# Performance work log

Measured on AMD Instinct MI355X. Metric: run time of the kernel, lower is better.

Reference implementation:

```python
import jax, jax.numpy as jnp
import numpy as np


def _dnn(a, b):
    # tf.math.divide_no_nan
    safe = jnp.where(b == 0, 1.0, b)
    return jnp.where(b == 0, 0.0, a / safe)


def _safe_sqrt(x):
    # _sqrt: 0 where x == 0 (grad-safe)
    p = x > 0
    return jnp.where(p, jnp.sqrt(jnp.where(p, x, 1.0)), 0.0)


def _agg4(v):
    # mean/var/skew/kurt over last axis, using the sample skew/kurt formulas
    # from _skewness2/_kurtosis2 in the source.
    n = float(v.shape[-1])
    m = jnp.mean(v, -1)
    c = v - m[..., None]
    var = jnp.mean(c ** 2, -1)
    std = _safe_sqrt(var)
    skew = n / ((n - 1.0) * (n - 2.0)) * jnp.sum(_dnn(c, std[..., None]) ** 3, -1)
    k4 = jnp.sum(c ** 4, -1)
    k22 = jnp.sum(c ** 2, -1) ** 2
    alpha = n * (n + 1.0) * (n - 1.0) / (n - 2.0) / (n - 3.0)
    kurt = alpha * _dnn(k4, k22) - 3.0 * (n - 1.0) ** 2 / (n - 2.0) / (n - 3.0)
    return m, var, skew, kurt


def _forward(x):
    B, T, F = x.shape
    nT = float(T)

    mean = jnp.mean(x, 1)                        # [B,F]
    xc = x - mean[:, None, :]                    # x_sub_means
    var = jnp.mean(xc ** 2, 1)                   # population variance
    std = _safe_sqrt(var)
    # diff: conv kernel [0,1,-1] VALID -> d[t] = x[t+1] - x[t+2], len T-2
    xd = x[:, 1:-1, :] - x[:, 2:, :]
    xd_abs = jnp.abs(xd)

    scal = [mean,
            jnp.min(x, 1), jnp.max(x, 1),
            _safe_sqrt(jnp.mean(x ** 2, 1)),      # rms
            var, std]
    # skewness / kurtosis over time (exact formulas from source)
    skew = nT / ((nT - 1.0) * (nT - 2.0)) * jnp.sum(_dnn(xc, std[:, None, :]) ** 3, 1)
    k4 = jnp.sum(xc ** 4, 1)
    k22 = jnp.sum(xc ** 2, 1) ** 2
    alpha = nT * (nT + 1.0) * (nT - 1.0) / (nT - 2.0) / (nT - 3.0)
    kurt = alpha * _dnn(k4, k22) - 3.0 * (nT - 1.0) ** 2 / (nT - 2.0) / (nT - 3.0)
    scal += [skew, kurt,
             jnp.mean(xd, 1), jnp.sum(xd, 1), jnp.mean(xd_abs, 1),  # change stats
             jnp.sum(x ** 2, 1),                  # abs_energy
             jnp.max(jnp.abs(x), 1),              # abs_max
             jnp.sum(xd_abs, 1),                  # abs_sum_of_changes
             _safe_sqrt(jnp.sum(xd ** 2, 1))]     # cid_ce

    # quantiles (sorted) and time-based quantiles
    xs = jnp.sort(x, axis=1)
    q_idx = [round(p * T) for p in (0.25, 0.5, 0.75)]
    q = xs[:, q_idx, :]                           # [B,3,F]
    tb_idx = [min(round(p * T), T - 1) for p in (0.0, 0.25, 0.5, 0.75, 1.0)]
    tb = x[:, tb_idx, :]                          # [B,5,F]

    def count_above(sgn):
        # count_above_zero: T - count_nonzero(sign - 1) == #(sign == 1)
        return jnp.sum(sgn == 1, 1).astype(x.dtype)

    def crossings(sgn):
        return jnp.sum(sgn[:, 1:, :] != sgn[:, :-1, :], 1).astype(x.dtype)

    s_x = jnp.sign(x)
    s_c = jnp.sign(xc)
    s_tb = [jnp.sign(x - tb[:, i:i + 1, :]) for i in range(5)]
    s_q = [jnp.sign(x - q[:, i:i + 1, :]) for i in range(3)]

    scal += [count_above(s_x), count_above(s_c)] + [count_above(s) for s in s_tb]
    scal += [crossings(s_x), crossings(s_c)]
    scal += [crossings(s) for s in s_q]
    scal += [crossings(s) for s in s_tb]

    # FFT features
    fx = jnp.fft.rfft(x, axis=1)                  # [B, T//2+1, F]
    amp = jnp.transpose(jnp.abs(fx), (0, 2, 1))   # [B,F,nf]
    ang = jnp.transpose(jnp.angle(fx), (0, 2, 1))
    ratio = _dnn(amp, jnp.sum(amp, -1, keepdims=True))
    am, av, ask, aku = _agg4(amp)
    rm, rv, rsk, rku = _agg4(ratio)
    scal += [amp[:, :, 0], am, av, ask, aku, rm, rv, rsk, rku]

    # autocorrelation (lags 1..9), matching _autocorrelation:
    # ac[l] = sum_t xc[t]*xc[t+l] / (T - l) / variance
    lags = list(range(1, 10))
    ac = jnp.stack([_dnn(jnp.sum(xc[:, :T - l, :] * xc[:, l:, :], 1) / (nT - l), var)
                    for l in lags], axis=-1)      # [B,F,9]
    acm, acv, acs, ack = _agg4(ac)
    ac_rmax = _dnn(ac, jnp.max(ac, -1, keepdims=True))
    scal += [acm, acv, acs, ack]

    out = jnp.concatenate(
        [jnp.stack(scal, -1),                     # [B,F,45]
         jnp.transpose(q, (0, 2, 1)),             # [B,F,3]
         jnp.transpose(tb, (0, 2, 1)),            # [B,F,5]
         amp, ang, ratio,                         # [B,F,1025] each
         ac, ac_rmax], axis=-1)                   # [B,F,9] each
    return out                                    # [B,F,3146]


def setup_inputs() -> dict:
    key = jax.random.key(0)
    x = jax.random.normal(key, (512, 2048, 16), dtype=jnp.float32)
    return {"x": x}


def reference(x):
    return _forward(x)
```

## Files before the change

### kernel.cpp

```cpp
#include <hip/hip_runtime.h>
#include <math.h>

#define T_LEN 2048
#define NF    16
#define NTH   256
#define NOUT  3146
#define PI_F  3.14159265358979323846f

__device__ __forceinline__ float wred_sum(float v) {
  v += __shfl_down(v, 32); v += __shfl_down(v, 16); v += __shfl_down(v, 8);
  v += __shfl_down(v, 4);  v += __shfl_down(v, 2);  v += __shfl_down(v, 1);
  return v;
}
__device__ __forceinline__ float wred_min(float v) {
  v = fminf(v, __shfl_down(v, 32)); v = fminf(v, __shfl_down(v, 16)); v = fminf(v, __shfl_down(v, 8));
  v = fminf(v, __shfl_down(v, 4));  v = fminf(v, __shfl_down(v, 2));  v = fminf(v, __shfl_down(v, 1));
  return v;
}
__device__ __forceinline__ float wred_max(float v) {
  v = fmaxf(v, __shfl_down(v, 32)); v = fmaxf(v, __shfl_down(v, 16)); v = fmaxf(v, __shfl_down(v, 8));
  v = fmaxf(v, __shfl_down(v, 4));  v = fmaxf(v, __shfl_down(v, 2));  v = fmaxf(v, __shfl_down(v, 1));
  return v;
}

template<int N>
__device__ __forceinline__ void block_sum_n(float (&v)[N], float* redw, float* res, int tid) {
  const int wave = tid >> 6;
#pragma unroll
  for (int j = 0; j < N; j++) {
    float s = wred_sum(v[j]);
    if ((tid & 63) == 0) redw[j * 4 + wave] = s;
  }
  __syncthreads();
  if (tid < N) res[tid] = redw[tid * 4] + redw[tid * 4 + 1] + redw[tid * 4 + 2] + redw[tid * 4 + 3];
  __syncthreads();
}

__device__ __forceinline__ void agg4_9(const float* v, float* om, float* ov, float* os, float* ok) {
  const float fn = 9.0f;
  float s = 0.f;
#pragma unroll
  for (int i = 0; i < 9; i++) s += v[i];
  float m = s / fn;
  float c2 = 0.f, c3 = 0.f, c4 = 0.f;
#pragma unroll
  for (int i = 0; i < 9; i++) {
    float c = v[i] - m; float cc = c * c;
    c2 += cc; c3 += cc * c; c4 += cc * cc;
  }
  float var = c2 / fn;
  float sd = (var > 0.f) ? sqrtf(var) : 0.f;
  float sk = (sd > 0.f) ? fn / ((fn - 1.f) * (fn - 2.f)) * (c3 / (sd * sd * sd)) : 0.f;
  float k22 = c2 * c2;
  float al = fn * (fn + 1.f) * (fn - 1.f) / ((fn - 2.f) * (fn - 3.f));
  float ku = ((k22 > 0.f) ? al * c4 / k22 : 0.f)
             - 3.f * (fn - 1.f) * (fn - 1.f) / ((fn - 2.f) * (fn - 3.f));
  *om = m; *ov = var; *os = sk; *ok = ku;
}

__device__ __forceinline__ void hist_scan(unsigned int* U, int tid) {
  if (tid < 64) {
    const int l = tid;
    unsigned int b0 = U[4*l]   + U[256+4*l]   + U[512+4*l]   + U[768+4*l];
    unsigned int b1 = U[4*l+1] + U[256+4*l+1] + U[512+4*l+1] + U[768+4*l+1];
    unsigned int b2 = U[4*l+2] + U[256+4*l+2] + U[512+4*l+2] + U[768+4*l+2];
    unsigned int b3 = U[4*l+3] + U[256+4*l+3] + U[512+4*l+3] + U[768+4*l+3];
    unsigned int s0 = b0, s1 = s0+b1, s2 = s1+b2, s3 = s2+b3;
    unsigned int tot = s3;
#pragma unroll
    for (int off = 1; off < 64; off <<= 1) {
      unsigned int n = __shfl_up(tot, off);
      if (l >= off) tot += n;
    }
    unsigned int base = tot - s3;
    U[1024+4*l] = base+s0; U[1024+4*l+1] = base+s1; U[1024+4*l+2] = base+s2; U[1024+4*l+3] = base+s3;
  }
  __syncthreads();
}

__device__ __forceinline__ void hist_scan3(unsigned int* U, int tid) {
  if (tid < 192) {
    int w = tid >> 6, l = tid & 63;
    unsigned int* h = U + w * 256;
    unsigned int b0 = h[4*l], b1 = h[4*l+1], b2 = h[4*l+2], b3 = h[4*l+3];
    unsigned int s0 = b0, s1 = s0+b1, s2 = s1+b2, s3 = s2+b3;
    unsigned int tot = s3;
#pragma unroll
    for (int off = 1; off < 64; off <<= 1) {
      unsigned int n = __shfl_up(tot, off);
      if (l >= off) tot += n;
    }
    unsigned int base = tot - s3;
    unsigned int* c = U + 768 + w * 256;
    c[4*l] = base+s0; c[4*l+1] = base+s1; c[4*l+2] = base+s2; c[4*l+3] = base+s3;
  }
  __syncthreads();
}

__device__ __forceinline__ float ord2f(unsigned int u) {
  unsigned int v = (u & 0x80000000u) ? (u ^ 0x80000000u) : ~u;
  return __uint_as_float(v);
}

__device__ __forceinline__ float fast_atan2f(float y, float x) {
  float ay = fabsf(y), ax = fabsf(x);
  float mx = fmaxf(ax, ay), mn = fminf(ax, ay);
  if (mx == 0.f) return 0.f;
  float t = __fdividef(mn, mx);
  float s = t * t;
  float p = fmaf(s, fmaf(s, fmaf(s, fmaf(s, 0.0208351f, -0.0851330f), 0.1801410f), -0.3302995f), 0.9998660f);
  float r = t * p;
  if (ay > ax) r = 1.57079632679f - r;
  if (x < 0.f) r = PI_F - r;
  return (y < 0.f) ? -r : r;
}

__global__ __launch_bounds__(NTH)
void ts_feat_kernel(const float* __restrict__ x, float* __restrict__ out, int gpx) {
  __shared__ __align__(16) float a[T_LEN];
  __shared__ __align__(16) float zr[1024];
  __shared__ __align__(16) float zi[1024];
  __shared__ __align__(16) unsigned int U[1536];
  __shared__ float redw[80];
  __shared__ float res[24];
  __shared__ float scal[48];
  __shared__ unsigned int selres[8];

  const int tid = threadIdx.x;
  int b, f;
  {
    int i = blockIdx.x;
    if (gpx > 0) { int xc = i & 7; int slot = i >> 3; b = xc * gpx + (slot >> 4); f = slot & 15; }
    else { b = i >> 4; f = i & 15; }
  }
  const float* xp = x + ((size_t)b * T_LEN) * NF + f;
  float* op = out + (size_t)(b * NF + f) * NOUT;
  const float fT = (float)T_LEN;

  float mean, S2v, MN, MX;
  {
    float s1 = 0.f, s2 = 0.f, mn = 3.4e38f, mx = -3.4e38f;
#pragma unroll
    for (int k = 0; k < 8; k++) {
      int t = tid + k * NTH;
      float v = xp[(size_t)t * NF];
      a[t] = v;
      s1 += v; s2 += v * v; mn = fminf(mn, v); mx = fmaxf(mx, v);
    }
    s1 = wred_sum(s1); s2 = wred_sum(s2); mn = wred_min(mn); mx = wred_max(mx);
    if ((tid & 63) == 0) { int w = tid >> 6; redw[w] = s1; redw[4+w] = s2; redw[8+w] = mn; redw[12+w] = mx; }
    __syncthreads();
    if (tid == 0) {
      res[0] = redw[0]+redw[1]+redw[2]+redw[3];
      res[1] = redw[4]+redw[5]+redw[6]+redw[7];
      res[2] = fminf(fminf(redw[8], redw[9]), fminf(redw[10], redw[11]));
      res[3] = fmaxf(fmaxf(redw[12], redw[13]), fmaxf(redw[14], redw[15]));
    }
    __syncthreads();
    mean = res[0] / fT; S2v = res[1]; MN = res[2]; MX = res[3];
  }
  float maxabs = fmaxf(-MN, MX);
  float rms = sqrtf(fmaxf(S2v / fT, 0.f));

  float var, sd, skw, kurt, SD, SAD, SDD;
  float ac[9], acm, acv, acs, ack, acmax;
  {
    const int base = tid * 8;
    const float4* a4 = (const float4*)a;
    float4 w0 = a4[tid*2], w1 = a4[tid*2+1];
    int i2 = (base + 11 < T_LEN) ? tid*2+2 : 0;
    int i3 = (base + 15 < T_LEN) ? tid*2+3 : 0;
    float4 w2 = a4[i2], w3 = a4[i3];
    bool ok2 = (base + 11 < T_LEN), ok3 = (base + 15 < T_LEN);
    float r[17];
    r[0]=w0.x; r[1]=w0.y; r[2]=w0.z; r[3]=w0.w;
    r[4]=w1.x; r[5]=w1.y; r[6]=w1.z; r[7]=w1.w;
    r[8]  = ok2 ? w2.x : mean; r[9]  = ok2 ? w2.y : mean; r[10] = ok2 ? w2.z : mean; r[11] = ok2 ? w2.w : mean;
    r[12] = ok3 ? w3.x : mean; r[13] = ok3 ? w3.y : mean; r[14] = ok3 ? w3.z : mean; r[15] = ok3 ? w3.w : mean;
    r[16] = (base + 16 < T_LEN) ? a[base + 16] : mean;

    float v15[15];
#pragma unroll
    for (int j = 0; j < 15; j++) v15[j] = 0.f;
#pragma unroll
    for (int j = 0; j < 8; j++) {
      float c = r[j] - mean; float cc = c * c;
      v15[0] += cc; v15[1] += cc * c; v15[2] += cc * cc;
    }
#pragma unroll
    for (int j = 0; j < 8; j++) {
      if (base + j < T_LEN - 2) {
        float d = r[j+1] - r[j+2];
        v15[3] += d; v15[4] += fabsf(d); v15[5] += d * d;
      }
    }
#pragma unroll
    for (int l = 1; l <= 9; l++) {
#pragma unroll
      for (int j = 0; j < 8; j++) {
        v15[5 + l] += (r[j] - mean) * (r[j + l] - mean);
      }
    }
    block_sum_n<15>(v15, redw, res, tid);
    float C2 = res[0], C3 = res[1], C4 = res[2];
    SD = res[3]; SAD = res[4]; SDD = res[5];
    var = C2 / fT;
    sd = (var > 0.f) ? sqrtf(var) : 0.f;
    skw = (sd > 0.f) ? (fT / ((fT - 1.f) * (fT - 2.f))) * (C3 / (sd * sd * sd)) : 0.f;
    float k22 = C2 * C2;
    float alphaT = fT * (fT + 1.f) * (fT - 1.f) / ((fT - 2.f) * (fT - 3.f));
    kurt = ((k22 > 0.f) ? alphaT * C4 / k22 : 0.f)
           - 3.f * (fT - 1.f) * (fT - 1.f) / ((fT - 2.f) * (fT - 3.f));
    float invvar = (var != 0.f) ? 1.f / var : 0.f;
#pragma unroll
    for (int l = 1; l <= 9; l++) ac[l-1] = res[5 + l] / (fT - (float)l) * invvar;
    agg4_9(ac, &acm, &acv, &acs, &ack);
    acmax = ac[0];
#pragma unroll
    for (int l = 1; l < 9; l++) acmax = fmaxf(acmax, ac[l]);
  }

  float q0, q1, q2;
  {
    unsigned int key[8];
#pragma unroll
    for (int k = 0; k < 8; k++) {
      unsigned int u = __float_as_uint(a[tid + k * NTH]);
      key[k] = (u & 0x80000000u) ? ~u : (u | 0x80000000u);
    }
    unsigned int prefix[3] = {0u, 0u, 0u};
    unsigned int rank[3] = {512u, 1024u, 1536u};
    const int woff = (tid >> 6) << 8;

    for (int q = tid; q < 1280; q += NTH) U[q] = 0u;
    __syncthreads();
#pragma unroll
    for (int k = 0; k < 8; k++) atomicAdd(&U[woff + (key[k] >> 24)], 1u);
    __syncthreads();
    hist_scan(U, tid);
    if (tid < 256) {
      unsigned int incl = U[1024 + tid];
      unsigned int excl = (tid == 0) ? 0u : U[1024 + tid - 1];
#pragma unroll
      for (int j = 0; j < 3; j++)
        if (excl <= rank[j] && rank[j] < incl) { selres[2*j] = (unsigned)tid; selres[2*j+1] = rank[j] - excl; }
    }
    __syncthreads();
#pragma unroll
    for (int j = 0; j < 3; j++) { prefix[j] = selres[2*j] << 24; rank[j] = selres[2*j+1]; }
    __syncthreads();

    for (int rnd = 1; rnd < 4; rnd++) {
      const int shift = 24 - 8 * rnd;
      for (int q = tid; q < 1536; q += NTH) U[q] = 0u;
      __syncthreads();
#pragma unroll
      for (int k = 0; k < 8; k++) {
        unsigned int u = key[k];
        unsigned int hi = u >> (shift + 8);
#pragma unroll
        for (int j = 0; j < 3; j++) {
          if (hi == (prefix[j] >> (shift + 8)))
            atomicAdd(&U[j * 256 + ((u >> shift) & 255u)], 1u);
        }
      }
      __syncthreads();
      hist_scan3(U, tid);
      if (tid < 192) {
        int j = tid >> 6, l = tid & 63;
#pragma unroll
        for (int i = 0; i < 4; i++) {
          int bk = 4 * l + i;
          unsigned int incl = U[768 + j * 256 + bk];
          unsigned int excl = (bk == 0) ? 0u : U[768 + j * 256 + bk - 1];
          if (excl <= rank[j] && rank[j] < incl) { selres[2*j] = (unsigned)bk; selres[2*j+1] = rank[j] - excl; }
        }
      }
      __syncthreads();
#pragma unroll
      for (int j = 0; j < 3; j++) { prefix[j] |= selres[2*j] << shift; rank[j] = selres[2*j+1]; }
      if (rnd < 3) __syncthreads();
    }
    q0 = ord2f(prefix[0]); q1 = ord2f(prefix[1]); q2 = ord2f(prefix[2]);
  }

  float tb0 = a[0], tb1 = a[512], tb2 = a[1024], tb3 = a[1536], tb4 = a[2047];

  float CNT0, CNT1, CNT5, CNT6, CNT7, CNT8, CNT9;
  float CRS0, CRS1, CRS2, CRS3, CRS4, CRS5, CRS6, CRS7, CRS8, CRS9;
  {
    const int base = tid * 8;
    const float4* a4 = (const float4*)a;
    float4 w0 = a4[tid*2], w1 = a4[tid*2+1];
    float rr[9];
    rr[0]=w0.x; rr[1]=w0.y; rr[2]=w0.z; rr[3]=w0.w;
    rr[4]=w1.x; rr[5]=w1.y; rr[6]=w1.z; rr[7]=w1.w;
    rr[8] = (base + 8 < T_LEN) ? a[base + 8] : 0.f;
    float v20[20];
#pragma unroll
    for (int j = 0; j < 20; j++) v20[j] = 0.f;
#pragma unroll
    for (int j = 0; j < 8; j++) {
      float v = rr[j], vn = rr[j + 1];
      bool hn = (base + j) < (T_LEN - 1);
#define THR_ONE(J, TH)                                            \
      { float d = v - (TH); int s = (d > 0.f) - (d < 0.f);        \
        v20[J] += (s == 1) ? 1.f : 0.f;                           \
        if (hn) { float dn = vn - (TH); int sn = (dn > 0.f) - (dn < 0.f); \
          v20[10 + J] += (s != sn) ? 1.f : 0.f; } }
      THR_ONE(0, 0.f)  THR_ONE(1, mean) THR_ONE(2, q0)  THR_ONE(3, q1)  THR_ONE(4, q2)
      THR_ONE(5, tb0)  THR_ONE(6, tb1)  THR_ONE(7, tb2) THR_ONE(8, tb3) THR_ONE(9, tb4)
#undef THR_ONE
    }
    block_sum_n<20>(v20, redw, res, tid);
    CNT0 = res[0]; CNT1 = res[1];
    CNT5 = res[5]; CNT6 = res[6]; CNT7 = res[7]; CNT8 = res[8]; CNT9 = res[9];
    CRS0 = res[10]; CRS1 = res[11]; CRS2 = res[12]; CRS3 = res[13]; CRS4 = res[14];
    CRS5 = res[15]; CRS6 = res[16]; CRS7 = res[17]; CRS8 = res[18]; CRS9 = res[19];
  }

  float amp0, amp1, amp2, amp3, amp4 = 0.f, S, invS;
  {
    float* Uf = (float*)U;
#pragma unroll
    for (int k = 0; k < 2; k++) {
      int p = tid + k * NTH;
      float sn, cs;
      __sincosf(-PI_F / 512.f * (float)p, &sn, &cs);
      int qx = p ^ (p >> 5);
      Uf[qx] = cs; Uf[512 + qx] = sn;
    }
    const float2* a2 = (const float2*)a;
#pragma unroll
    for (int k = 0; k < 4; k++) {
      int p = tid + k * NTH;
      float2 z = a2[p];
      int rl = (int)(__brev((unsigned)(p & 31)) >> 27);
      int c = p >> 5;
      int idx = rl * 32 + (c ^ rl);
      zr[idx] = z.x; zi[idx] = z.y;
    }
    __syncthreads();
    float gr[4], gi[4];
#pragma unroll
    for (int k = 0; k < 4; k++) {
      int m = tid + k * NTH;
      int h = m >> 5, l = m & 31;
      int rl5 = (int)(__brev((unsigned)l) >> 27);
      int idx = h * 32 + (rl5 ^ h);
      gr[k] = zr[idx]; gi[k] = zi[idx];
    }
    __syncthreads();
#pragma unroll
    for (int k = 0; k < 4; k++) { int m = tid + k * NTH; zr[m] = gr[k]; zi[m] = gi[k]; }
    for (int s = 1; s <= 10; s++) {
      const int hf = 1 << (s - 1);
      const int tsh = 10 - s;
      __syncthreads();
#pragma unroll
      for (int jj = 0; jj < 2; jj++) {
        int m = tid + (jj << 8);
        int pos = m & (hf - 1);
        int i0 = ((m >> (s - 1)) << s) | pos;
        int i1 = i0 + hf;
        int p = pos << tsh;
        int tix = p ^ (p >> 5);
        float cs = Uf[tix], sn = Uf[512 + tix];
        float xr = zr[i1], xi = zi[i1];
        float tr = cs * xr - sn * xi;
        float ti = cs * xi + sn * xr;
        float ur = zr[i0], ui = zi[i0];
        zr[i0] = ur + tr; zi[i0] = ui + ti;
        zr[i1] = ur - tr; zi[i1] = ui - ti;
      }
    }
    __syncthreads();

    float samp = 0.f;
    float ampv[4];
#pragma unroll
    for (int k = 0; k < 4; k++) {
      int kk = tid + k * NTH;
      int nk = (1024 - kk) & 1023;
      float z1r = zr[kk], z1i = zi[kk];
      float z2r = zr[nk], z2i = zi[nk];
      float Er = 0.5f * (z1r + z2r), Ei = 0.5f * (z1i - z2i);
      float Or = 0.5f * (z1i + z2i), Oi = -0.5f * (z1r - z2r);
      float sn, cs;
      __sincosf(-PI_F * (float)kk * (1.f / 1024.f), &sn, &cs);
      float Xr = Er + cs * Or - sn * Oi;
      float Xi = Ei + cs * Oi + sn * Or;
      float amp = sqrtf(Xr * Xr + Xi * Xi);
      float ang = fast_atan2f(Xi, Xr);
      op[53 + kk] = amp;
      op[1078 + kk] = ang;
      a[kk] = amp;
      samp += amp;
      ampv[k] = amp;
    }
    amp0 = ampv[0]; amp1 = ampv[1]; amp2 = ampv[2]; amp3 = ampv[3];
    if (tid == 0) {
      float Xr = zr[0] - zi[0];
      float amp = fabsf(Xr);
      op[53 + 1024] = amp;
      op[1078 + 1024] = (Xr < 0.f) ? PI_F : 0.f;
      a[1024] = amp;
      samp += amp;
      amp4 = amp;
    }
    float v1[1] = {samp};
    block_sum_n<1>(v1, redw, res, tid);
    S = res[0];
    invS = (S != 0.f) ? 1.f / S : 0.f;
    op[2103 + tid]       = amp0 * invS;
    op[2103 + tid + 256] = amp1 * invS;
    op[2103 + tid + 512] = amp2 * invS;
    op[2103 + tid + 768] = amp3 * invS;
    if (tid == 0) op[2103 + 1024] = amp4 * invS;
  }

  const float fn = 1025.f;
  float am = S / fn;
  float av, ask, aku, rm, rv;
  {
    float c0 = amp0 - am, c1 = amp1 - am, c2 = amp2 - am, c3 = amp3 - am;
    float c4 = (tid == 0) ? (amp4 - am) : 0.f;
    float v3[3];
    v3[0] = c0*c0 + c1*c1 + c2*c2 + c3*c3 + c4*c4;
    v3[1] = c0*c0*c0 + c1*c1*c1 + c2*c2*c2 + c3*c3*c3 + c4*c4*c4;
    v3[2] = c0*c0*c0*c0 + c1*c1*c1*c1 + c2*c2*c2*c2 + c3*c3*c3*c3 + c4*c4*c4*c4;
    block_sum_n<3>(v3, redw, res, tid);
    float A2 = res[0], A3 = res[1], A4 = res[2];
    av = A2 / fn;
    float asd = (av > 0.f) ? sqrtf(av) : 0.f;
    ask = (asd > 0.f) ? fn / ((fn - 1.f) * (fn - 2.f)) * (A3 / (asd * asd * asd)) : 0.f;
    float ak22 = A2 * A2;
    float aal = fn * (fn + 1.f) * (fn - 1.f) / ((fn - 2.f) * (fn - 3.f));
    aku = ((ak22 > 0.f) ? aal * A4 / ak22 : 0.f)
          - 3.f * (fn - 1.f) * (fn - 1.f) / ((fn - 2.f) * (fn - 3.f));
    rm = am * invS;
    rv = av * invS * invS;
  }

  if (tid == 0) {
    scal[0] = mean; scal[1] = MN; scal[2] = MX; scal[3] = rms; scal[4] = var; scal[5] = sd;
    scal[6] = skw; scal[7] = kurt;
    scal[8] = SD / (fT - 2.f); scal[9] = SD; scal[10] = SAD / (fT - 2.f);
    scal[11] = S2v; scal[12] = maxabs; scal[13] = SAD;
    scal[14] = (SDD > 0.f) ? sqrtf(SDD) : 0.f;
    scal[15] = CNT0; scal[16] = CNT1;
    scal[17] = CNT5; scal[18] = CNT6; scal[19] = CNT7; scal[20] = CNT8; scal[21] = CNT9;
    scal[22] = CRS0; scal[23] = CRS1;
    scal[24] = CRS2; scal[25] = CRS3; scal[26] = CRS4;
    scal[27] = CRS5; scal[28] = CRS6; scal[29] = CRS7; scal[30] = CRS8; scal[31] = CRS9;
    scal[32] = a[0];
    scal[33] = am; scal[34] = av; scal[35] = ask; scal[36] = aku;
    scal[37] = rm; scal[38] = rv; scal[39] = ask; scal[40] = aku;
    scal[41] = acm; scal[42] = acv; scal[43] = acs; scal[44] = ack;
    scal[45] = q0; scal[46] = q1; scal[47] = q2;
  }
  __syncthreads();
  if (tid < 48) op[tid] = scal[tid];
  if (tid == 0) {
    op[48] = tb0; op[49] = tb1; op[50] = tb2; op[51] = tb3; op[52] = tb4;
  }
  if (tid < 9) {
    float acj;
    switch (tid) {
      case 0: acj = ac[0]; break; case 1: acj = ac[1]; break; case 2: acj = ac[2]; break;
      case 3: acj = ac[3]; break; case 4: acj = ac[4]; break; case 5: acj = ac[5]; break;
      case 6: acj = ac[6]; break; case 7: acj = ac[7]; break; default: acj = ac[8]; break;
    }
    op[3128 + tid] = acj;
    op[3137 + tid] = (acmax != 0.f) ? acj / acmax : 0.f;
  }
}

extern "C" void kernel_launch(void* const* d_in, const int* in_sizes, int n_in,
                              void* d_out, int out_size, void* d_ws, size_t ws_size,
                              hipStream_t stream) {
  const float* x = (const float*)d_in[0];
  float* out = (float*)d_out;
  const int total = in_sizes[0];
  const int B = total / (T_LEN * NF);
  const int nblocks = B * NF;
  const int gpx = (B % 8 == 0) ? (B / 8) : 0;
  ts_feat_kernel<<<nblocks, NTH, 0, stream>>>(x, out, gpx);
}
```

Measured before the change: 243.7 us.

## Use wave ballots for threshold counts and radix-4 FFT stages

Threshold-count and crossing statistics are now computed with wave-wide ballot and popcount over register-held samples, with a small seam pass between waves, instead of per-thread float accumulation and a 20-value block reduction. The 10 radix-2 FFT stages are replaced by 5 radix-4 stages, which halves the number of barriers and shared-memory passes. Input samples are kept in registers so the quantile search and the counting reuse them without re-reading shared memory, and the amplitude write-back into shared memory is dropped. In exchange the crossing logic now depends on how time indices map to lanes, which is less obvious to check, and register pressure rises.

Measured after the change: 254.8 us. +4.5%, slower.

```diff
diff --git a/kernel.cpp b/kernel.cpp
--- a/kernel.cpp
+++ b/kernel.cpp
@@ -100,6 +100,10 @@
 __device__ __forceinline__ float ord2f(unsigned int u) {
   unsigned int v = (u & 0x80000000u) ? (u ^ 0x80000000u) : ~u;
   return __uint_as_float(v);
+}
+__device__ __forceinline__ unsigned int f2ord(float v) {
+  unsigned int u = __float_as_uint(v);
+  return (u & 0x80000000u) ? ~u : (u | 0x80000000u);
 }
 
 __device__ __forceinline__ float fast_atan2f(float y, float x) {
@@ -121,7 +125,7 @@
   __shared__ __align__(16) float zr[1024];
   __shared__ __align__(16) float zi[1024];
   __shared__ __align__(16) unsigned int U[1536];
-  __shared__ float redw[80];
+  __shared__ float redw[96];
   __shared__ float res[24];
   __shared__ float scal[48];
   __shared__ unsigned int selres[8];
@@ -136,7 +140,9 @@
   const float* xp = x + ((size_t)b * T_LEN) * NF + f;
   float* op = out + (size_t)(b * NF + f) * NOUT;
   const float fT = (float)T_LEN;
-
+  const int lane = tid & 63;
+
+  float xv[8];
   float mean, S2v, MN, MX;
   {
     float s1 = 0.f, s2 = 0.f, mn = 3.4e38f, mx = -3.4e38f;
@@ -144,11 +150,12 @@
     for (int k = 0; k < 8; k++) {
       int t = tid + k * NTH;
       float v = xp[(size_t)t * NF];
+      xv[k] = v;
       a[t] = v;
       s1 += v; s2 += v * v; mn = fminf(mn, v); mx = fmaxf(mx, v);
     }
     s1 = wred_sum(s1); s2 = wred_sum(s2); mn = wred_min(mn); mx = wred_max(mx);
-    if ((tid & 63) == 0) { int w = tid >> 6; redw[w] = s1; redw[4+w] = s2; redw[8+w] = mn; redw[12+w] = mx; }
+    if (lane == 0) { int w = tid >> 6; redw[w] = s1; redw[4+w] = s2; redw[8+w] = mn; redw[12+w] = mx; }
     __syncthreads();
     if (tid == 0) {
       res[0] = redw[0]+redw[1]+redw[2]+redw[3];
@@ -222,12 +229,6 @@
 
   float q0, q1, q2;
   {
-    unsigned int key[8];
-#pragma unroll
-    for (int k = 0; k < 8; k++) {
-      unsigned int u = __float_as_uint(a[tid + k * NTH]);
-      key[k] = (u & 0x80000000u) ? ~u : (u | 0x80000000u);
-    }
     unsigned int prefix[3] = {0u, 0u, 0u};
     unsigned int rank[3] = {512u, 1024u, 1536u};
     const int woff = (tid >> 6) << 8;
@@ -235,7 +236,7 @@
     for (int q = tid; q < 1280; q += NTH) U[q] = 0u;
     __syncthreads();
 #pragma unroll
-    for (int k = 0; k < 8; k++) atomicAdd(&U[woff + (key[k] >> 24)], 1u);
+    for (int k = 0; k < 8; k++) atomicAdd(&U[woff + (f2ord(xv[k]) >> 24)], 1u);
     __syncthreads();
     hist_scan(U, tid);
     if (tid < 256) {
@@ -256,7 +257,7 @@
       __syncthreads();
 #pragma unroll
       for (int k = 0; k < 8; k++) {
-        unsigned int u = key[k];
+        unsigned int u = f2ord(xv[k]);
         unsigned int hi = u >> (shift + 8);
 #pragma unroll
         for (int j = 0; j < 3; j++) {
@@ -289,30 +290,61 @@
   float CNT0, CNT1, CNT5, CNT6, CNT7, CNT8, CNT9;
   float CRS0, CRS1, CRS2, CRS3, CRS4, CRS5, CRS6, CRS7, CRS8, CRS9;
   {
-    const int base = tid * 8;
-    const float4* a4 = (const float4*)a;
-    float4 w0 = a4[tid*2], w1 = a4[tid*2+1];
-    float rr[9];
-    rr[0]=w0.x; rr[1]=w0.y; rr[2]=w0.z; rr[3]=w0.w;
-    rr[4]=w1.x; rr[5]=w1.y; rr[6]=w1.z; rr[7]=w1.w;
-    rr[8] = (base + 8 < T_LEN) ? a[base + 8] : 0.f;
-    float v20[20];
-#pragma unroll
-    for (int j = 0; j < 20; j++) v20[j] = 0.f;
-#pragma unroll
-    for (int j = 0; j < 8; j++) {
-      float v = rr[j], vn = rr[j + 1];
-      bool hn = (base + j) < (T_LEN - 1);
-#define THR_ONE(J, TH)                                            \
-      { float d = v - (TH); int s = (d > 0.f) - (d < 0.f);        \
-        v20[J] += (s == 1) ? 1.f : 0.f;                           \
-        if (hn) { float dn = vn - (TH); int sn = (dn > 0.f) - (dn < 0.f); \
-          v20[10 + J] += (s != sn) ? 1.f : 0.f; } }
-      THR_ONE(0, 0.f)  THR_ONE(1, mean) THR_ONE(2, q0)  THR_ONE(3, q1)  THR_ONE(4, q2)
-      THR_ONE(5, tb0)  THR_ONE(6, tb1)  THR_ONE(7, tb2) THR_ONE(8, tb3) THR_ONE(9, tb4)
-#undef THR_ONE
-    }
-    block_sum_n<20>(v20, redw, res, tid);
+    const float th0 = 0.f, th1 = mean, th2 = q0, th3 = q1, th4 = q2;
+    const float th5 = tb0, th6 = tb1, th7 = tb2, th8 = tb3, th9 = tb4;
+    int cnt0=0,cnt1=0,cnt2=0,cnt3=0,cnt4=0,cnt5=0,cnt6=0,cnt7=0,cnt8=0,cnt9=0;
+    int crs0=0,crs1=0,crs2=0,crs3=0,crs4=0,crs5=0,crs6=0,crs7=0,crs8=0,crs9=0;
+#pragma unroll
+    for (int k = 0; k < 8; k++) {
+      float v = xv[k];
+#define BAL(J, TH)                                                        \
+      { unsigned long long mp = __ballot(v > (TH));                       \
+        unsigned long long mz = __ballot(v == (TH));                      \
+        cnt##J += (int)__popcll(mp);                                      \
+        unsigned long long df = ((mp ^ (mp >> 1)) | (mz ^ (mz >> 1)))     \
+                                & 0x7fffffffffffffffull;                  \
+        crs##J += (int)__popcll(df); }
+      BAL(0, th0) BAL(1, th1) BAL(2, th2) BAL(3, th3) BAL(4, th4)
+      BAL(5, th5) BAL(6, th6) BAL(7, th7) BAL(8, th8) BAL(9, th9)
+#undef BAL
+    }
+    if (tid < 64) {
+      float cse[10];
+      bool act = (tid < 31);
+      float a0 = act ? a[64*tid + 63] : 0.f;
+      float a1 = act ? a[64*tid + 64] : 0.f;
+#define SEAM(J, TH)                                                       \
+      { bool g0 = a0 > (TH), g1 = a1 > (TH);                              \
+        bool e0 = a0 == (TH), e1 = a1 == (TH);                            \
+        cse[J] = (act && ((g0 != g1) || (e0 != e1))) ? 1.f : 0.f; }
+      SEAM(0, th0) SEAM(1, th1) SEAM(2, th2) SEAM(3, th3) SEAM(4, th4)
+      SEAM(5, th5) SEAM(6, th6) SEAM(7, th7) SEAM(8, th8) SEAM(9, th9)
+#undef SEAM
+#pragma unroll
+      for (int j = 0; j < 10; j++) cse[j] = wred_sum(cse[j]);
+      if (tid == 0) {
+#pragma unroll
+        for (int j = 0; j < 10; j++) redw[80 + j] = cse[j];
+      }
+    }
+    if (lane == 0) {
+      int w = tid >> 6;
+      redw[w*20+0]=(float)cnt0; redw[w*20+1]=(float)cnt1; redw[w*20+2]=(float)cnt2;
+      redw[w*20+3]=(float)cnt3; redw[w*20+4]=(float)cnt4; redw[w*20+5]=(float)cnt5;
+      redw[w*20+6]=(float)cnt6; redw[w*20+7]=(float)cnt7; redw[w*20+8]=(float)cnt8;
+      redw[w*20+9]=(float)cnt9;
+      redw[w*20+10]=(float)crs0; redw[w*20+11]=(float)crs1; redw[w*20+12]=(float)crs2;
+      redw[w*20+13]=(float)crs3; redw[w*20+14]=(float)crs4; redw[w*20+15]=(float)crs5;
+      redw[w*20+16]=(float)crs6; redw[w*20+17]=(float)crs7; redw[w*20+18]=(float)crs8;
+      redw[w*20+19]=(float)crs9;
+    }
+    __syncthreads();
+    if (tid < 20) {
+      float s = redw[tid] + redw[20+tid] + redw[40+tid] + redw[60+tid];
+      if (tid >= 10) s += redw[80 + (tid - 10)];
+      res[tid] = s;
+    }
+    __syncthreads();
     CNT0 = res[0]; CNT1 = res[1];
     CNT5 = res[5]; CNT6 = res[6]; CNT7 = res[7]; CNT8 = res[8]; CNT9 = res[9];
     CRS0 = res[10]; CRS1 = res[11]; CRS2 = res[12]; CRS3 = res[13]; CRS4 = res[14];
@@ -353,25 +385,49 @@
     __syncthreads();
 #pragma unroll
     for (int k = 0; k < 4; k++) { int m = tid + k * NTH; zr[m] = gr[k]; zi[m] = gi[k]; }
-    for (int s = 1; s <= 10; s++) {
-      const int hf = 1 << (s - 1);
-      const int tsh = 10 - s;
+
+#pragma unroll
+    for (int p = 0; p < 5; p++) {
+      const int hf = 1 << (2 * p);
       __syncthreads();
-#pragma unroll
-      for (int jj = 0; jj < 2; jj++) {
-        int m = tid + (jj << 8);
-        int pos = m & (hf - 1);
-        int i0 = ((m >> (s - 1)) << s) | pos;
-        int i1 = i0 + hf;
-        int p = pos << tsh;
-        int tix = p ^ (p >> 5);
-        float cs = Uf[tix], sn = Uf[512 + tix];
-        float xr = zr[i1], xi = zi[i1];
-        float tr = cs * xr - sn * xi;
-        float ti = cs * xi + sn * xr;
-        float ur = zr[i0], ui = zi[i0];
-        zr[i0] = ur + tr; zi[i0] = ui + ti;
-        zr[i1] = ur - tr; zi[i1] = ui - ti;
+      if (p == 0) {
+        float4 R = ((const float4*)zr)[tid];
+        float4 I = ((const float4*)zi)[tid];
+        float u0r = R.x + R.y, u0i = I.x + I.y;
+        float u1r = R.x - R.y, u1i = I.x - I.y;
+        float u2r = R.z + R.w, u2i = I.z + I.w;
+        float u3r = R.z - R.w, u3i = I.z - I.w;
+        float4 Ro, Io;
+        Ro.x = u0r + u2r; Io.x = u0i + u2i;
+        Ro.z = u0r - u2r; Io.z = u0i - u2i;
+        Ro.y = u1r + u3i; Io.y = u1i - u3r;
+        Ro.w = u1r - u3i; Io.w = u1i + u3r;
+        ((float4*)zr)[tid] = Ro; ((float4*)zi)[tid] = Io;
+      } else {
+        const int q = tid & (hf - 1);
+        const int i0 = ((tid >> (2 * p)) << (2 * p + 2)) | q;
+        const int i1 = i0 + hf, i2 = i0 + 2 * hf, i3 = i0 + 3 * hf;
+        const int t1 = q << (9 - 2 * p);
+        const int t2 = q << (8 - 2 * p);
+        const int t3 = t2 + 256;
+        const int x1 = t1 ^ (t1 >> 5), x2 = t2 ^ (t2 >> 5), x3 = t3 ^ (t3 >> 5);
+        float c1 = Uf[x1], s1 = Uf[512 + x1];
+        float c2 = Uf[x2], s2 = Uf[512 + x2];
+        float c3 = Uf[x3], s3 = Uf[512 + x3];
+        float r0 = zr[i0], m0 = zi[i0], r1 = zr[i1], m1 = zi[i1];
+        float r2 = zr[i2], m2 = zi[i2], r3 = zr[i3], m3 = zi[i3];
+        float a1r = c1*r1 - s1*m1, a1i = c1*m1 + s1*r1;
+        float a3r = c1*r3 - s1*m3, a3i = c1*m3 + s1*r3;
+        float u0r = r0 + a1r, u0i = m0 + a1i;
+        float u1r = r0 - a1r, u1i = m0 - a1i;
+        float u2r = r2 + a3r, u2i = m2 + a3i;
+        float u3r = r2 - a3r, u3i = m2 - a3i;
+        float b2r = c2*u2r - s2*u2i, b2i = c2*u2i + s2*u2r;
+        float b3r = c3*u3r - s3*u3i, b3i = c3*u3i + s3*u3r;
+        zr[i0] = u0r + b2r; zi[i0] = u0i + b2i;
+        zr[i2] = u0r - b2r; zi[i2] = u0i - b2i;
+        zr[i1] = u1r + b3r; zi[i1] = u1i + b3i;
+        zr[i3] = u1r - b3r; zi[i3] = u1i - b3i;
       }
     }
     __syncthreads();
@@ -394,7 +450,6 @@
       float ang = fast_atan2f(Xi, Xr);
       op[53 + kk] = amp;
       op[1078 + kk] = ang;
-      a[kk] = amp;
       samp += amp;
       ampv[k] = amp;
     }
@@ -404,7 +459,6 @@
       float amp = fabsf(Xr);
       op[53 + 1024] = amp;
       op[1078 + 1024] = (Xr < 0.f) ? PI_F : 0.f;
-      a[1024] = amp;
       samp += amp;
       amp4 = amp;
     }
@@ -453,7 +507,7 @@
     scal[22] = CRS0; scal[23] = CRS1;
     scal[24] = CRS2; scal[25] = CRS3; scal[26] = CRS4;
     scal[27] = CRS5; scal[28] = CRS6; scal[29] = CRS7; scal[30] = CRS8; scal[31] = CRS9;
-    scal[32] = a[0];
+    scal[32] = amp0;
     scal[33] = am; scal[34] = av; scal[35] = ask; scal[36] = aku;
     scal[37] = rm; scal[38] = rv; scal[39] = ask; scal[40] = aku;
     scal[41] = acm; scal[42] = acv; scal[43] = acs; scal[44] = ack;
```
